# Performance work log

Measured on AMD Instinct MI355X. Metric: run time of the kernel, lower is better.

Reference implementation:

```python
import jax, jax.numpy as jnp
import numpy as np

B, S, N = 8, 2048, 1024

def setup_inputs() -> dict:
    key = jax.random.key(0)
    k1, k2, k3 = jax.random.split(key, 3)
    outer = jax.random.normal(k1, (B, S, N), dtype=jnp.float32)
    extended_attention_mask = jnp.zeros((B, 1, S), dtype=jnp.float32)
    # torch Linear init scale ~ 1/sqrt(n)
    sc = 1.0 / np.sqrt(N)
    Wk = jax.random.normal(k2, (N, N), dtype=jnp.float32) * sc
    bk = jnp.zeros((N,), dtype=jnp.float32)
    Wq = jax.random.normal(k3, (N, N), dtype=jnp.float32) * sc
    bq = jnp.zeros((N,), dtype=jnp.float32)
    return {"outer": outer, "extended_attention_mask": extended_attention_mask,
            "Wk": Wk, "bk": bk, "Wq": Wq, "bq": bq}

def reference(outer, extended_attention_mask, Wk, bk, Wq, bq):
    # k = sigmoid(outer @ Wk^T + bk), q = sigmoid(outer @ Wq^T + bq)
    k = jax.nn.sigmoid(jnp.einsum('bsn,mn->bsm', outer, Wk) + bk)  # [B,S,N]
    q = jax.nn.sigmoid(jnp.einsum('bsn,mn->bsm', outer, Wq) + bq)  # [B,S,N]
    # scores: q @ k^T + mask -> [B,S,S]
    s = jnp.einsum('bqn,bkn->bqk', q, k) + extended_attention_mask
    attn = jax.nn.softmax(s, axis=-1)
    out = jnp.einsum('bqk,bkn->bqn', attn, outer)  # [B,S,N]
    return out.sum(-1)  # [B,S]
```

## Files before the change

kernel.cpp:

```cpp
#include <hip/hip_runtime.h>
#include <hip/hip_bf16.h>

#define BB 8
#define SS 2048
#define NN 1024
#define MT (BB*SS)
#define NKC 16

typedef __attribute__((ext_vector_type(8))) short bf16x8;
typedef __attribute__((ext_vector_type(4))) float f32x4;
typedef unsigned short u16;
typedef unsigned int u32;

__device__ __forceinline__ u16 f2bf(float f) {
  u32 u = __float_as_uint(f);
  u += 0x7fff + ((u >> 16) & 1);
  return (u16)(u >> 16);
}
__device__ __forceinline__ float bf2f(u16 h) {
  return __uint_as_float(((u32)h) << 16);
}

typedef __attribute__((address_space(1))) void GV;
typedef __attribute__((address_space(3))) void LV;
__device__ __forceinline__ void cp16(const void* g, void* l) {
  __builtin_amdgcn_global_load_lds((GV*)g, (LV*)l, 16, 0, 0);
}

__global__ __launch_bounds__(256) void prep_x_kernel(const float* __restrict__ outer,
                                                     u16* __restrict__ Xb,
                                                     float* __restrict__ r) {
  int row = blockIdx.x;
  int tid = threadIdx.x;
  const float4* src = (const float4*)(outer + (size_t)row * NN);
  float4 v = src[tid];
  ushort4 o;
  o.x = f2bf(v.x); o.y = f2bf(v.y); o.z = f2bf(v.z); o.w = f2bf(v.w);
  ((ushort4*)(Xb + (size_t)row * NN))[tid] = o;
  float s = (v.x + v.y) + (v.z + v.w);
  for (int off = 32; off > 0; off >>= 1) s += __shfl_down(s, off);
  __shared__ float red[4];
  int w = tid >> 6, lane = tid & 63;
  if (lane == 0) red[w] = s;
  __syncthreads();
  if (tid == 0) r[row] = (red[0] + red[1]) + (red[2] + red[3]);
}

__global__ __launch_bounds__(256) void prep_w_kernel(const float* __restrict__ Wq,
                                                     const float* __restrict__ Wk,
                                                     const float* __restrict__ bq,
                                                     const float* __restrict__ bk,
                                                     u16* __restrict__ Wb,
                                                     float* __restrict__ bb) {
  int idx = blockIdx.x * 256 + threadIdx.x;
  int e = idx * 4;
  int rowm = e >> 10;
  int col = e & 1023;
  const float* srcp = (rowm < NN) ? (Wq + (size_t)rowm * NN + col)
                                  : (Wk + (size_t)(rowm - NN) * NN + col);
  float4 v = *(const float4*)srcp;
  ushort4 o; o.x = f2bf(v.x); o.y = f2bf(v.y); o.z = f2bf(v.z); o.w = f2bf(v.w);
  *(ushort4*)(Wb + (size_t)e) = o;
  if (idx < 2 * NN) bb[idx] = (idx < NN) ? bq[idx] : bk[idx - NN];
}

__global__ __launch_bounds__(256, 3) void gemm1_kernel(const u16* __restrict__ X,
                                                       const u16* __restrict__ W,
                                                       const float* __restrict__ bb,
                                                       u16* __restrict__ C) {
  __shared__ u16 lA[128 * 32];
  __shared__ u16 lB[128 * 32];
  int tn = blockIdx.x;
  int tm = blockIdx.y;
  int tid = threadIdx.x;
  int w = tid >> 6, lane = tid & 63;
  int srow = tid >> 2;
  int scol = (tid & 3) * 8;
  const u16* gA = X + (size_t)(tm * 128 + srow) * NN + scol;
  const u16* gB = W + (size_t)(tn * 128 + srow) * NN + scol;
  u16* dA = &lA[srow * 32 + scol];
  u16* dB = &lB[srow * 32 + scol];
  const u16* pa0 = &lA[(w * 32 + (lane & 15)) * 32 + (lane >> 4) * 8];
  const u16* pb0 = &lB[(lane & 15) * 32 + (lane >> 4) * 8];
  f32x4 acc[2][8] = {};
  for (int kk = 0; kk < NN; kk += 32) {
    cp16(gA, dA);
    cp16(gA + 64 * NN, dA + 64 * 32);
    cp16(gB, dB);
    cp16(gB + 64 * NN, dB + 64 * 32);
    gA += 32; gB += 32;
    __syncthreads();
    bf16x8 a0 = *(const bf16x8*)(pa0);
    bf16x8 a1 = *(const bf16x8*)(pa0 + 16 * 32);
#pragma unroll
    for (int j = 0; j < 8; j++) {
      bf16x8 bfrag = *(const bf16x8*)(pb0 + j * 16 * 32);
      acc[0][j] = __builtin_amdgcn_mfma_f32_16x16x32_bf16(a0, bfrag, acc[0][j], 0, 0, 0);
      acc[1][j] = __builtin_amdgcn_mfma_f32_16x16x32_bf16(a1, bfrag, acc[1][j], 0, 0, 0);
    }
    __syncthreads();
  }
  int quad = lane >> 4;
  int colb = tn * 128 + (lane & 15);
#pragma unroll
  for (int i = 0; i < 2; i++) {
#pragma unroll
    for (int j = 0; j < 8; j++) {
      int col = colb + j * 16;
      float bias = bb[col];
#pragma unroll
      for (int rg = 0; rg < 4; rg++) {
        int row = tm * 128 + w * 32 + i * 16 + quad * 4 + rg;
        float v = acc[i][j][rg] + bias;
        float sg = 1.0f / (1.0f + __expf(-v));
        C[(size_t)row * 2048 + col] = f2bf(sg - 0.5f);
      }
    }
  }
}

__global__ __launch_bounds__(256) void kbias_kernel(const u16* __restrict__ C,
                                                    const float* __restrict__ mask,
                                                    float* __restrict__ kb) {
  int row = blockIdx.x;
  int tid = threadIdx.x;
  ushort4 u = ((const ushort4*)(C + (size_t)row * 2048 + 1024))[tid];
  float s = (bf2f(u.x) + bf2f(u.y)) + (bf2f(u.z) + bf2f(u.w));
  for (int off = 32; off > 0; off >>= 1) s += __shfl_down(s, off);
  __shared__ float red[4];
  int w = tid >> 6, lane = tid & 63;
  if (lane == 0) red[w] = s;
  __syncthreads();
  if (tid == 0) kb[row] = 0.5f * ((red[0] + red[1]) + (red[2] + red[3])) + mask[row];
}

__global__ __launch_bounds__(256, 3) void flash_kernel(const u16* __restrict__ C,
                                                       const float* __restrict__ kb,
                                                       const float* __restrict__ r,
                                                       float* __restrict__ pm,
                                                       float* __restrict__ pl,
                                                       float* __restrict__ pt) {
  __shared__ u16 lA[128 * 32];
  __shared__ u16 lB[128 * 32];
  int bid = blockIdx.x;
  int kc = bid & 15;
  int qt = (bid >> 4) & 15;
  int b  = bid >> 8;
  int tid = threadIdx.x;
  int w = tid >> 6, lane = tid & 63;
  int srow = tid >> 2;
  int scol = (tid & 3) * 8;
  int key0 = kc * 128;
  const u16* gA = C + (size_t)(b * SS + qt * 128 + srow) * 2048 + scol;
  const u16* gB = C + (size_t)(b * SS + key0 + srow) * 2048 + 1024 + scol;
  u16* dA = &lA[srow * 32 + scol];
  u16* dB = &lB[srow * 32 + scol];
  const u16* pa0 = &lA[(w * 32 + (lane & 15)) * 32 + (lane >> 4) * 8];
  const u16* pb0 = &lB[(lane & 15) * 32 + (lane >> 4) * 8];
  int quad = lane >> 4;

  f32x4 acc[2][8] = {};
  for (int kk = 0; kk < NN; kk += 32) {
    cp16(gA, dA);
    cp16(gA + 64 * 2048, dA + 64 * 32);
    cp16(gB, dB);
    cp16(gB + 64 * 2048, dB + 64 * 32);
    gA += 32; gB += 32;
    __syncthreads();
    bf16x8 a0 = *(const bf16x8*)(pa0);
    bf16x8 a1 = *(const bf16x8*)(pa0 + 16 * 32);
#pragma unroll
    for (int j = 0; j < 8; j++) {
      bf16x8 bfrag = *(const bf16x8*)(pb0 + j * 16 * 32);
      acc[0][j] = __builtin_amdgcn_mfma_f32_16x16x32_bf16(a0, bfrag, acc[0][j], 0, 0, 0);
      acc[1][j] = __builtin_amdgcn_mfma_f32_16x16x32_bf16(a1, bfrag, acc[1][j], 0, 0, 0);
    }
    __syncthreads();
  }

  float kbv[8], rv[8];
  int colg = b * SS + key0 + (lane & 15);
#pragma unroll
  for (int j = 0; j < 8; j++) { kbv[j] = kb[colg + j * 16]; rv[j] = r[colg + j * 16]; }
#pragma unroll
  for (int i = 0; i < 2; i++) {
#pragma unroll
    for (int rg = 0; rg < 4; rg++) {
      float lg[8];
      float tmax = -1e30f;
#pragma unroll
      for (int j = 0; j < 8; j++) { lg[j] = acc[i][j][rg] + kbv[j]; tmax = fmaxf(tmax, lg[j]); }
#pragma unroll
      for (int off = 1; off < 16; off <<= 1) tmax = fmaxf(tmax, __shfl_xor(tmax, off));
      float rs = 0.f, rt = 0.f;
#pragma unroll
      for (int j = 0; j < 8; j++) {
        float p = __expf(lg[j] - tmax);
        rs += p; rt += p * rv[j];
      }
#pragma unroll
      for (int off = 1; off < 16; off <<= 1) { rs += __shfl_xor(rs, off); rt += __shfl_xor(rt, off); }
      if ((lane & 15) == 0) {
        int grow = b * SS + qt * 128 + w * 32 + i * 16 + quad * 4 + rg;
        pm[grow * NKC + kc] = tmax;
        pl[grow * NKC + kc] = rs;
        pt[grow * NKC + kc] = rt;
      }
    }
  }
}

__global__ __launch_bounds__(256) void fixup_kernel(const float* __restrict__ pm,
                                                    const float* __restrict__ pl,
                                                    const float* __restrict__ pt,
                                                    float* __restrict__ out) {
  int row = blockIdx.x * 256 + threadIdx.x;
  float Mx = -1e30f;
#pragma unroll
  for (int c = 0; c < NKC; c++) Mx = fmaxf(Mx, pm[row * NKC + c]);
  float L = 0.f, T = 0.f;
#pragma unroll
  for (int c = 0; c < NKC; c++) {
    float a = __expf(pm[row * NKC + c] - Mx);
    L += pl[row * NKC + c] * a;
    T += pt[row * NKC + c] * a;
  }
  out[row] = T / L;
}

extern "C" void kernel_launch(void* const* d_in, const int* in_sizes, int n_in,
                              void* d_out, int out_size, void* d_ws, size_t ws_size,
                              hipStream_t stream) {
  const float* outer = (const float*)d_in[0];
  const float* mask  = (const float*)d_in[1];
  const float* Wk    = (const float*)d_in[2];
  const float* bk    = (const float*)d_in[3];
  const float* Wq    = (const float*)d_in[4];
  const float* bq    = (const float*)d_in[5];
  float* out = (float*)d_out;

  char* ws = (char*)d_ws;
  size_t off = 0;
  auto alloc = [&](size_t bytes) -> void* {
    void* p = ws + off;
    off = (off + bytes + 255) & ~(size_t)255;
    return p;
  };
  u16* Xb  = (u16*)alloc((size_t)MT * NN * 2);
  u16* Wb  = (u16*)alloc((size_t)2048 * NN * 2);
  u16* Cq  = (u16*)alloc((size_t)MT * 2048 * 2);
  float* bb = (float*)alloc(2048 * 4);
  float* rr = (float*)alloc((size_t)MT * 4);
  float* kb = (float*)alloc((size_t)MT * 4);
  float* pm = (float*)alloc((size_t)MT * NKC * 4);
  float* pl = (float*)alloc((size_t)MT * NKC * 4);
  float* pt = (float*)alloc((size_t)MT * NKC * 4);

  prep_x_kernel<<<dim3(MT), dim3(256), 0, stream>>>(outer, Xb, rr);
  prep_w_kernel<<<dim3(2048), dim3(256), 0, stream>>>(Wq, Wk, bq, bk, Wb, bb);
  gemm1_kernel<<<dim3(16, 128), dim3(256), 0, stream>>>(Xb, Wb, bb, Cq);
  kbias_kernel<<<dim3(MT), dim3(256), 0, stream>>>(Cq, mask, kb);
  flash_kernel<<<dim3(8 * 16 * NKC), dim3(256), 0, stream>>>(Cq, kb, rr, pm, pl, pt);
  fixup_kernel<<<dim3(MT / 256), dim3(256), 0, stream>>>(pm, pl, pt, out);
}
```

Before: 300.9 us.

## Use 2x2 warp tiling in GEMMs and one row per wave in row reductions

Both MFMA kernels change from a 4x1 warp layout (each wave computing 32x128) to a 2x2 layout (each wave computing 64x64). This cuts LDS fragment loads per k-step from 10 to 8 per wave for the same 16 MFMAs. The flash epilogue now writes 32 partial softmax chunks per row instead of 16, so fixup reads twice as many partials. The prep_x and kbias kernels now handle one row per wavefront with shuffle-only reductions, removing shared memory and __syncthreads.

```diff
diff --git a/kernel.cpp b/kernel.cpp
--- a/kernel.cpp
+++ b/kernel.cpp
@@ -6,6 +6,7 @@
 #define NN 1024
 #define MT (BB*SS)
 #define NKC 16
+#define NPC 32
 
 typedef __attribute__((ext_vector_type(8))) short bf16x8;
 typedef __attribute__((ext_vector_type(4))) float f32x4;
@@ -30,20 +31,23 @@
 __global__ __launch_bounds__(256) void prep_x_kernel(const float* __restrict__ outer,
                                                      u16* __restrict__ Xb,
                                                      float* __restrict__ r) {
-  int row = blockIdx.x;
-  int tid = threadIdx.x;
+  int w = threadIdx.x >> 6, lane = threadIdx.x & 63;
+  int row = blockIdx.x * 4 + w;
   const float4* src = (const float4*)(outer + (size_t)row * NN);
-  float4 v = src[tid];
-  ushort4 o;
-  o.x = f2bf(v.x); o.y = f2bf(v.y); o.z = f2bf(v.z); o.w = f2bf(v.w);
-  ((ushort4*)(Xb + (size_t)row * NN))[tid] = o;
-  float s = (v.x + v.y) + (v.z + v.w);
-  for (int off = 32; off > 0; off >>= 1) s += __shfl_down(s, off);
-  __shared__ float red[4];
-  int w = tid >> 6, lane = tid & 63;
-  if (lane == 0) red[w] = s;
-  __syncthreads();
-  if (tid == 0) r[row] = (red[0] + red[1]) + (red[2] + red[3]);
+  ushort4* dst = (ushort4*)(Xb + (size_t)row * NN);
+  float s = 0.f;
+#pragma unroll
+  for (int u = 0; u < 4; u++) {
+    int idx = lane + u * 64;
+    float4 v = src[idx];
+    ushort4 o;
+    o.x = f2bf(v.x); o.y = f2bf(v.y); o.z = f2bf(v.z); o.w = f2bf(v.w);
+    dst[idx] = o;
+    s += (v.x + v.y) + (v.z + v.w);
+  }
+#pragma unroll
+  for (int off = 1; off < 64; off <<= 1) s += __shfl_xor(s, off);
+  if (lane == 0) r[row] = s;
 }
 
 __global__ __launch_bounds__(256) void prep_w_kernel(const float* __restrict__ Wq,
@@ -74,15 +78,17 @@
   int tm = blockIdx.y;
   int tid = threadIdx.x;
   int w = tid >> 6, lane = tid & 63;
+  int wr = w >> 1, wc = w & 1;
   int srow = tid >> 2;
   int scol = (tid & 3) * 8;
   const u16* gA = X + (size_t)(tm * 128 + srow) * NN + scol;
   const u16* gB = W + (size_t)(tn * 128 + srow) * NN + scol;
   u16* dA = &lA[srow * 32 + scol];
   u16* dB = &lB[srow * 32 + scol];
-  const u16* pa0 = &lA[(w * 32 + (lane & 15)) * 32 + (lane >> 4) * 8];
-  const u16* pb0 = &lB[(lane & 15) * 32 + (lane >> 4) * 8];
-  f32x4 acc[2][8] = {};
+  int quad = lane >> 4;
+  const u16* pa0 = &lA[(wr * 64 + (lane & 15)) * 32 + quad * 8];
+  const u16* pb0 = &lB[(wc * 64 + (lane & 15)) * 32 + quad * 8];
+  f32x4 acc[4][4] = {};
   for (int kk = 0; kk < NN; kk += 32) {
     cp16(gA, dA);
     cp16(gA + 64 * NN, dA + 64 * 32);
@@ -90,27 +96,29 @@
     cp16(gB + 64 * NN, dB + 64 * 32);
     gA += 32; gB += 32;
     __syncthreads();
-    bf16x8 a0 = *(const bf16x8*)(pa0);
-    bf16x8 a1 = *(const bf16x8*)(pa0 + 16 * 32);
-#pragma unroll
-    for (int j = 0; j < 8; j++) {
-      bf16x8 bfrag = *(const bf16x8*)(pb0 + j * 16 * 32);
-      acc[0][j] = __builtin_amdgcn_mfma_f32_16x16x32_bf16(a0, bfrag, acc[0][j], 0, 0, 0);
-      acc[1][j] = __builtin_amdgcn_mfma_f32_16x16x32_bf16(a1, bfrag, acc[1][j], 0, 0, 0);
-    }
-    __syncthreads();
-  }
-  int quad = lane >> 4;
-  int colb = tn * 128 + (lane & 15);
-#pragma unroll
-  for (int i = 0; i < 2; i++) {
-#pragma unroll
-    for (int j = 0; j < 8; j++) {
+    bf16x8 af[4], bf[4];
+#pragma unroll
+    for (int i = 0; i < 4; i++) af[i] = *(const bf16x8*)(pa0 + i * 16 * 32);
+#pragma unroll
+    for (int j = 0; j < 4; j++) bf[j] = *(const bf16x8*)(pb0 + j * 16 * 32);
+#pragma unroll
+    for (int i = 0; i < 4; i++)
+#pragma unroll
+      for (int j = 0; j < 4; j++)
+        acc[i][j] = __builtin_amdgcn_mfma_f32_16x16x32_bf16(af[i], bf[j], acc[i][j], 0, 0, 0);
+    __syncthreads();
+  }
+  int quad4 = quad * 4;
+  int colb = tn * 128 + wc * 64 + (lane & 15);
+#pragma unroll
+  for (int i = 0; i < 4; i++) {
+#pragma unroll
+    for (int j = 0; j < 4; j++) {
       int col = colb + j * 16;
       float bias = bb[col];
 #pragma unroll
       for (int rg = 0; rg < 4; rg++) {
-        int row = tm * 128 + w * 32 + i * 16 + quad * 4 + rg;
+        int row = tm * 128 + wr * 64 + i * 16 + quad4 + rg;
         float v = acc[i][j][rg] + bias;
         float sg = 1.0f / (1.0f + __expf(-v));
         C[(size_t)row * 2048 + col] = f2bf(sg - 0.5f);
@@ -122,16 +130,18 @@
 __global__ __launch_bounds__(256) void kbias_kernel(const u16* __restrict__ C,
                                                     const float* __restrict__ mask,
                                                     float* __restrict__ kb) {
-  int row = blockIdx.x;
-  int tid = threadIdx.x;
-  ushort4 u = ((const ushort4*)(C + (size_t)row * 2048 + 1024))[tid];
-  float s = (bf2f(u.x) + bf2f(u.y)) + (bf2f(u.z) + bf2f(u.w));
-  for (int off = 32; off > 0; off >>= 1) s += __shfl_down(s, off);
-  __shared__ float red[4];
-  int w = tid >> 6, lane = tid & 63;
-  if (lane == 0) red[w] = s;
-  __syncthreads();
-  if (tid == 0) kb[row] = 0.5f * ((red[0] + red[1]) + (red[2] + red[3])) + mask[row];
+  int w = threadIdx.x >> 6, lane = threadIdx.x & 63;
+  int row = blockIdx.x * 4 + w;
+  const ushort4* src = (const ushort4*)(C + (size_t)row * 2048 + 1024);
+  float s = 0.f;
+#pragma unroll
+  for (int u = 0; u < 4; u++) {
+    ushort4 v = src[lane + u * 64];
+    s += (bf2f(v.x) + bf2f(v.y)) + (bf2f(v.z) + bf2f(v.w));
+  }
+#pragma unroll
+  for (int off = 1; off < 64; off <<= 1) s += __shfl_xor(s, off);
+  if (lane == 0) kb[row] = 0.5f * s + mask[row];
 }
 
 __global__ __launch_bounds__(256, 3) void flash_kernel(const u16* __restrict__ C,
@@ -148,6 +158,7 @@
   int b  = bid >> 8;
   int tid = threadIdx.x;
   int w = tid >> 6, lane = tid & 63;
+  int wr = w >> 1, wc = w & 1;
   int srow = tid >> 2;
   int scol = (tid & 3) * 8;
   int key0 = kc * 128;
@@ -155,11 +166,11 @@
   const u16* gB = C + (size_t)(b * SS + key0 + srow) * 2048 + 1024 + scol;
   u16* dA = &lA[srow * 32 + scol];
   u16* dB = &lB[srow * 32 + scol];
-  const u16* pa0 = &lA[(w * 32 + (lane & 15)) * 32 + (lane >> 4) * 8];
-  const u16* pb0 = &lB[(lane & 15) * 32 + (lane >> 4) * 8];
   int quad = lane >> 4;
-
-  f32x4 acc[2][8] = {};
+  const u16* pa0 = &lA[(wr * 64 + (lane & 15)) * 32 + quad * 8];
+  const u16* pb0 = &lB[(wc * 64 + (lane & 15)) * 32 + quad * 8];
+
+  f32x4 acc[4][4] = {};
   for (int kk = 0; kk < NN; kk += 32) {
     cp16(gA, dA);
     cp16(gA + 64 * 2048, dA + 64 * 32);
@@ -167,44 +178,48 @@
     cp16(gB + 64 * 2048, dB + 64 * 32);
     gA += 32; gB += 32;
     __syncthreads();
-    bf16x8 a0 = *(const bf16x8*)(pa0);
-    bf16x8 a1 = *(const bf16x8*)(pa0 + 16 * 32);
-#pragma unroll
-    for (int j = 0; j < 8; j++) {
-      bf16x8 bfrag = *(const bf16x8*)(pb0 + j * 16 * 32);
-      acc[0][j] = __builtin_amdgcn_mfma_f32_16x16x32_bf16(a0, bfrag, acc[0][j], 0, 0, 0);
-      acc[1][j] = __builtin_amdgcn_mfma_f32_16x16x32_bf16(a1, bfrag, acc[1][j], 0, 0, 0);
-    }
-    __syncthreads();
-  }
-
-  float kbv[8], rv[8];
-  int colg = b * SS + key0 + (lane & 15);
-#pragma unroll
-  for (int j = 0; j < 8; j++) { kbv[j] = kb[colg + j * 16]; rv[j] = r[colg + j * 16]; }
-#pragma unroll
-  for (int i = 0; i < 2; i++) {
+    bf16x8 af[4], bf[4];
+#pragma unroll
+    for (int i = 0; i < 4; i++) af[i] = *(const bf16x8*)(pa0 + i * 16 * 32);
+#pragma unroll
+    for (int j = 0; j < 4; j++) bf[j] = *(const bf16x8*)(pb0 + j * 16 * 32);
+#pragma unroll
+    for (int i = 0; i < 4; i++)
+#pragma unroll
+      for (int j = 0; j < 4; j++)
+        acc[i][j] = __builtin_amdgcn_mfma_f32_16x16x32_bf16(af[i], bf[j], acc[i][j], 0, 0, 0);
+    __syncthreads();
+  }
+
+  float kbv[4], rv[4];
+  int colg = b * SS + key0 + wc * 64 + (lane & 15);
+#pragma unroll
+  for (int j = 0; j < 4; j++) { kbv[j] = kb[colg + j * 16]; rv[j] = r[colg + j * 16]; }
+  int quad4 = quad * 4;
+  int chunk = kc * 2 + wc;
+#pragma unroll
+  for (int i = 0; i < 4; i++) {
 #pragma unroll
     for (int rg = 0; rg < 4; rg++) {
-      float lg[8];
+      float lg[4];
       float tmax = -1e30f;
 #pragma unroll
-      for (int j = 0; j < 8; j++) { lg[j] = acc[i][j][rg] + kbv[j]; tmax = fmaxf(tmax, lg[j]); }
+      for (int j = 0; j < 4; j++) { lg[j] = acc[i][j][rg] + kbv[j]; tmax = fmaxf(tmax, lg[j]); }
 #pragma unroll
       for (int off = 1; off < 16; off <<= 1) tmax = fmaxf(tmax, __shfl_xor(tmax, off));
       float rs = 0.f, rt = 0.f;
 #pragma unroll
-      for (int j = 0; j < 8; j++) {
+      for (int j = 0; j < 4; j++) {
         float p = __expf(lg[j] - tmax);
         rs += p; rt += p * rv[j];
       }
 #pragma unroll
       for (int off = 1; off < 16; off <<= 1) { rs += __shfl_xor(rs, off); rt += __shfl_xor(rt, off); }
       if ((lane & 15) == 0) {
-        int grow = b * SS + qt * 128 + w * 32 + i * 16 + quad * 4 + rg;
-        pm[grow * NKC + kc] = tmax;
-        pl[grow * NKC + kc] = rs;
-        pt[grow * NKC + kc] = rt;
+        int grow = b * SS + qt * 128 + wr * 64 + i * 16 + quad4 + rg;
+        pm[grow * NPC + chunk] = tmax;
+        pl[grow * NPC + chunk] = rs;
+        pt[grow * NPC + chunk] = rt;
       }
     }
   }
@@ -217,13 +232,13 @@
   int row = blockIdx.x * 256 + threadIdx.x;
   float Mx = -1e30f;
 #pragma unroll
-  for (int c = 0; c < NKC; c++) Mx = fmaxf(Mx, pm[row * NKC + c]);
+  for (int c = 0; c < NPC; c++) Mx = fmaxf(Mx, pm[row * NPC + c]);
   float L = 0.f, T = 0.f;
 #pragma unroll
-  for (int c = 0; c < NKC; c++) {
-    float a = __expf(pm[row * NKC + c] - Mx);
-    L += pl[row * NKC + c] * a;
-    T += pt[row * NKC + c] * a;
+  for (int c = 0; c < NPC; c++) {
+    float a = __expf(pm[row * NPC + c] - Mx);
+    L += pl[row * NPC + c] * a;
+    T += pt[row * NPC + c] * a;
   }
   out[row] = T / L;
 }
@@ -252,14 +267,14 @@
   float* bb = (float*)alloc(2048 * 4);
   float* rr = (float*)alloc((size_t)MT * 4);
   float* kb = (float*)alloc((size_t)MT * 4);
-  float* pm = (float*)alloc((size_t)MT * NKC * 4);
-  float* pl = (float*)alloc((size_t)MT * NKC * 4);
-  float* pt = (float*)alloc((size_t)MT * NKC * 4);
-
-  prep_x_kernel<<<dim3(MT), dim3(256), 0, stream>>>(outer, Xb, rr);
+  float* pm = (float*)alloc((size_t)MT * NPC * 4);
+  float* pl = (float*)alloc((size_t)MT * NPC * 4);
+  float* pt = (float*)alloc((size_t)MT * NPC * 4);
+
+  prep_x_kernel<<<dim3(MT / 4), dim3(256), 0, stream>>>(outer, Xb, rr);
   prep_w_kernel<<<dim3(2048), dim3(256), 0, stream>>>(Wq, Wk, bq, bk, Wb, bb);
   gemm1_kernel<<<dim3(16, 128), dim3(256), 0, stream>>>(Xb, Wb, bb, Cq);
-  kbias_kernel<<<dim3(MT), dim3(256), 0, stream>>>(Cq, mask, kb);
+  kbias_kernel<<<dim3(MT / 4), dim3(256), 0, stream>>>(Cq, mask, kb);
   flash_kernel<<<dim3(8 * 16 * NKC), dim3(256), 0, stream>>>(Cq, kb, rr, pm, pl, pt);
   fixup_kernel<<<dim3(MT / 256), dim3(256), 0, stream>>>(pm, pl, pt, out);
 }
```

New measurement: 307.5 us. +2.2%, slower.
